# Performance work log

Hardware: AMD Instinct MI355X
Metric: run time of the kernel (lower is better)

The kernel has to match this reference:

```python
import jax, jax.numpy as jnp
import numpy as np

N, E, B = 20000, 320000, 128
IN_DIM, HID, HEADS = 64, 64, 4
D = HID * HEADS          # 256 = conv output width (concat heads)
CAT = HID + 2 * D        # 576 = dueling head input
ENC_H, DUEL_H = 512, 128
NEG_SLOPE = 0.2


def setup_inputs() -> dict:
    key = jax.random.key(0)
    ks = jax.random.split(key, 30)
    g = lambda i, shape: jax.random.normal(ks[i], shape, dtype=jnp.float32) * 0.05
    return {
        "x": jax.random.normal(ks[0], (N, IN_DIM), dtype=jnp.float32),
        "edge_index": jax.random.randint(ks[1], (2, E), 0, N, dtype=jnp.int32),
        "indices": jax.random.randint(ks[2], (B,), 0, N, dtype=jnp.int32),
        # encoder MLP: input_dim -> 512 -> hidden_dim
        "enc_w1": g(3, (IN_DIM, ENC_H)), "enc_b1": g(4, (ENC_H,)),
        "enc_w2": g(5, (ENC_H, HID)),   "enc_b2": g(6, (HID,)),
        # GATv2 conv1: HID -> HID per head, HEADS heads
        "wl1": g(7, (HID, D)),  "bl1": g(8, (D,)),
        "wr1": g(9, (HID, D)),  "br1": g(10, (D,)),
        "att1": g(11, (HEADS, HID)), "bias1": g(12, (D,)),
        # GATv2 conv2: D -> HID per head, HEADS heads
        "wl2": g(13, (D, D)),   "bl2": g(14, (D,)),
        "wr2": g(15, (D, D)),   "br2": g(16, (D,)),
        "att2": g(17, (HEADS, HID)), "bias2": g(18, (D,)),
        # dueling heads: CAT -> 128 -> {2, 1}
        "q_w1": g(19, (CAT, DUEL_H)), "q_b1": g(20, (DUEL_H,)),
        "q_w2": g(21, (DUEL_H, 2)),   "q_b2": g(22, (2,)),
        "v_w1": g(23, (CAT, DUEL_H)), "v_b1": g(24, (DUEL_H,)),
        "v_w2": g(25, (DUEL_H, 1)),   "v_b2": g(26, (1,)),
    }


def _gatv2(h, src, dst, wl, bl, wr, br, att, bias):
    # PyG GATv2Conv: e_ij = att . leaky_relu(Wl h_j + Wr h_i); softmax over
    # incoming edges of each target i; out_i = sum_j alpha_ij * (Wl h_j).
    xl = (h @ wl + bl).reshape(-1, HEADS, HID)  # source transform
    xr = (h @ wr + br).reshape(-1, HEADS, HID)  # target transform
    e = jax.nn.leaky_relu(xl[src] + xr[dst], NEG_SLOPE)      # [E', H, D]
    score = jnp.einsum('ehd,hd->eh', e, att)                 # [E', H]
    m = jax.ops.segment_max(score, dst, num_segments=N)      # stable softmax
    ex = jnp.exp(score - m[dst])
    denom = jax.ops.segment_sum(ex, dst, num_segments=N)
    alpha = ex / (denom[dst] + 1e-16)                        # [E', H]
    out = jax.ops.segment_sum(alpha[:, :, None] * xl[src], dst, num_segments=N)
    return out.reshape(-1, D) + bias


def _forward(x, edge_index, indices,
             enc_w1, enc_b1, enc_w2, enc_b2,
             wl1, bl1, wr1, br1, att1, bias1,
             wl2, bl2, wr2, br2, att2, bias2,
             q_w1, q_b1, q_w2, q_b2, v_w1, v_b1, v_w2, v_b2):
    loops = jnp.arange(N, dtype=edge_index.dtype)  # add_self_loops=True
    src = jnp.concatenate([edge_index[0], loops])
    dst = jnp.concatenate([edge_index[1], loops])

    h = jax.nn.relu(x @ enc_w1 + enc_b1)
    h = jax.nn.relu(h @ enc_w2 + enc_b2)          # encoder + F.relu
    x1 = h[indices]
    h = jax.nn.relu(_gatv2(h, src, dst, wl1, bl1, wr1, br1, att1, bias1))
    x2 = h[indices]
    h = jax.nn.relu(_gatv2(h, src, dst, wl2, bl2, wr2, br2, att2, bias2))
    x3 = h[indices]

    feat = jnp.concatenate([x1, x2, x3], axis=1)  # [B, CAT]
    q = jax.nn.relu(feat @ q_w1 + q_b1) @ q_w2 + q_b2  # [B, 2]
    v = jax.nn.relu(feat @ v_w1 + v_b1) @ v_w2 + v_b2  # [B, 1]
    return q - q.mean(axis=1, keepdims=True) + v


def reference(x, edge_index, indices,
              enc_w1, enc_b1, enc_w2, enc_b2,
              wl1, bl1, wr1, br1, att1, bias1,
              wl2, bl2, wr2, br2, att2, bias2,
              q_w1, q_b1, q_w2, q_b2, v_w1, v_b1, v_w2, v_b2):
    return _forward(x, edge_index, indices,
                    enc_w1, enc_b1, enc_w2, enc_b2,
                    wl1, bl1, wr1, br1, att1, bias1,
                    wl2, bl2, wr2, br2, att2, bias2,
                    q_w1, q_b1, q_w2, q_b2, v_w1, v_b1, v_w2, v_b2)
```

## Files before the change

kernel.cpp:

```cpp
#include <hip/hip_runtime.h>

#define IN_DIM 64
#define HID 64
#define HEADS 4
#define DD 256
#define ENC_H 512
#define DUEL_H 128
#define NEG_SLOPE 0.2f
#define WCAP 8192
#define ECAP 64

typedef _Float16 f16;
typedef __attribute__((ext_vector_type(2))) _Float16 f16x2;
typedef __attribute__((ext_vector_type(4))) _Float16 f16x4;
typedef __attribute__((ext_vector_type(8))) _Float16 f16x8;
typedef __attribute__((ext_vector_type(4))) float f32x4;

__device__ __forceinline__ f16x2 u2h(unsigned u) {
    union { unsigned u; f16x2 h; } c; c.u = u; return c.h;
}
__device__ __forceinline__ unsigned h2u(f16x2 h) {
    union { unsigned u; f16x2 h; } c; c.h = h; return c.u;
}


__global__ void prep_all(
    const float4* __restrict__ x, f16x4* __restrict__ x16, int nx4,
    const float* __restrict__ w1, const float* __restrict__ w2,
    const float* __restrict__ wl1, const float* __restrict__ wr1,
    const float* __restrict__ wl2, const float* __restrict__ wr2,
    f16* __restrict__ w1t, f16* __restrict__ w2t,
    f16* __restrict__ wcat1, f16* __restrict__ wcat2,
    f16* __restrict__ wr2nt,
    int* __restrict__ zeros, int nz) {
    int i = blockIdx.x * blockDim.x + threadIdx.x;
    if (i < nx4) {
        float4 v = x[i];
        f16x4 o = {(f16)v.x, (f16)v.y, (f16)v.z, (f16)v.w};
        x16[i] = o;
        return;
    }
    i -= nx4;
    if (i < 229376) {
        if (i < 32768) {
            int k = i >> 9, n = i & 511;
            w1t[n * 64 + k] = (f16)w1[i];
        } else if (i < 65536) {
            int j = i - 32768; int k = j >> 6, n = j & 63;
            w2t[n * 512 + k] = (f16)w2[j];
        } else if (i < 81920) {
            int j = i - 65536; int k = j >> 8, n = j & 255;
            wcat1[n * 64 + k] = (f16)wl1[j];
        } else if (i < 98304) {
            int j = i - 81920; int k = j >> 8, n = j & 255;
            wcat1[(256 + n) * 64 + k] = (f16)wr1[j];
        } else if (i < 163840) {
            int j = i - 98304; int k = j >> 8, n = j & 255;
            wcat2[n * 256 + k] = (f16)wl2[j];
        } else {
            int j = i - 163840;
            wr2nt[j] = (f16)wr2[j];
        }
        return;
    }
    i -= 229376;
    if (i < nz) zeros[i] = 0;
}


template <int K, int BN>
struct GemmCfg {
    static constexpr int SB = K + 8;
    static constexpr int CE = BN / 2 + 8;
    static constexpr int SLABSZ = BN * SB;
    static constexpr int EPISZ = 4 * 32 * CE;
    static constexpr int SMEMSZ = SLABSZ > EPISZ ? SLABSZ : EPISZ;
};

template <int K, int BN>
__device__ __forceinline__ void gemm_body(
    int bx, int by, f16* __restrict__ smem,
    const f16* __restrict__ A, const f16* __restrict__ Bt,
    const float* __restrict__ biasA, const float* __restrict__ biasB, int NS,
    int M, int relu,
    f16* __restrict__ C1, f16* __restrict__ C2) {
    constexpr int KS = K / 32;
    constexpr int PF = (KS < 8) ? KS : 8;
    constexpr int COLW = BN / 2;
    constexpr int NT = COLW / 16;
    constexpr int SB = GemmCfg<K, BN>::SB;
    constexpr int CE = GemmCfg<K, BN>::CE;

    f16* Bs = smem;
    int tid = threadIdx.x;
    int wave = tid >> 6, lane = tid & 63;
    int quad = lane >> 4, l16 = lane & 15;
    int wr = wave >> 1, wc = wave & 1;
    int row0 = by * 64;
    int col0 = bx * BN;

    constexpr int NCH = BN * K / 8;
#pragma unroll
    for (int i = 0; i < NCH / 256; ++i) {
        int c = tid + i * 256;
        int r = c / (K / 8), ko = (c % (K / 8)) * 8;
        uint4 v = *(const uint4*)&Bt[(size_t)(col0 + r) * K + ko];
        *(uint4*)&Bs[r * SB + ko] = v;
    }
    __syncthreads();

    const f16* Aptr[2];
#pragma unroll
    for (int mt = 0; mt < 2; ++mt) {
        int arow = row0 + wr * 32 + mt * 16 + l16;
        if (arow >= M) arow = M - 1;
        Aptr[mt] = &A[(size_t)arow * K + quad * 8];
    }

    f32x4 acc[2][NT];
#pragma unroll
    for (int mt = 0; mt < 2; ++mt)
#pragma unroll
        for (int j = 0; j < NT; ++j) acc[mt][j] = (f32x4){0.f, 0.f, 0.f, 0.f};

    f16x8 afb[2][PF];
#pragma unroll
    for (int mt = 0; mt < 2; ++mt)
#pragma unroll
        for (int i = 0; i < PF; ++i)
            afb[mt][i] = *(const f16x8*)&Aptr[mt][i * 32];

#pragma unroll
    for (int s = 0; s < KS; ++s) {
        f16x8 af0 = afb[0][s % PF], af1 = afb[1][s % PF];
        if (s + PF < KS) {
            afb[0][s % PF] = *(const f16x8*)&Aptr[0][(s + PF) * 32];
            afb[1][s % PF] = *(const f16x8*)&Aptr[1][(s + PF) * 32];
        }
        const f16* bbase = &Bs[(size_t)(wc * COLW) * SB + s * 32 + quad * 8];
#pragma unroll
        for (int nt = 0; nt < NT; ++nt) {
            f16x8 bf = *(const f16x8*)&bbase[(nt * 16 + l16) * SB];
            acc[0][nt] = __builtin_amdgcn_mfma_f32_16x16x32_f16(af0, bf, acc[0][nt], 0, 0, 0);
            acc[1][nt] = __builtin_amdgcn_mfma_f32_16x16x32_f16(af1, bf, acc[1][nt], 0, 0, 0);
        }
    }

    __syncthreads();
    f16* ep = &smem[wave * 32 * CE];
#pragma unroll
    for (int mt = 0; mt < 2; ++mt)
#pragma unroll
        for (int nt = 0; nt < NT; ++nt) {
            int gcol = col0 + wc * COLW + nt * 16 + l16;
            float bb = (gcol < NS) ? biasA[gcol] : biasB[gcol - NS];
#pragma unroll
            for (int r = 0; r < 4; ++r) {
                float v = acc[mt][nt][r] + bb;
                if (relu) v = fmaxf(v, 0.f);
                ep[(mt * 16 + quad * 4 + r) * CE + nt * 16 + l16] = (f16)v;
            }
        }
    constexpr int CPR = COLW / 8;
    constexpr int NPASS = (32 * CPR) / 64;
#pragma unroll
    for (int i = 0; i < NPASS; ++i) {
        int u = lane + i * 64;
        int row = u / CPR, seg = u % CPR;
        uint4 v = *(const uint4*)&ep[row * CE + seg * 8];
        int grow = row0 + wr * 32 + row;
        int gcol = col0 + wc * COLW + seg * 8;
        if (grow < M) {
            if (gcol < NS) *(uint4*)&C1[(size_t)grow * NS + gcol] = v;
            else           *(uint4*)&C2[(size_t)grow * NS + (gcol - NS)] = v;
        }
    }
}


__global__ __launch_bounds__(256) void conv2t_gather_kernel(
    const f16* __restrict__ A, const f16* __restrict__ Bt,
    const float* __restrict__ bias,
    const int* __restrict__ wlist, const int* __restrict__ wcnt,
    f16* __restrict__ C) {
    constexpr int K = 256, BN = 128;
    constexpr int KS = K / 32, PF = 8;
    constexpr int COLW = BN / 2, NT = COLW / 16;
    constexpr int SB = GemmCfg<K, BN>::SB;
    constexpr int CE = GemmCfg<K, BN>::CE;
    __shared__ __align__(16) f16 smem[GemmCfg<K, BN>::SMEMSZ];

    int M_c = wcnt[0];
    int row0 = blockIdx.y * 64;
    if (row0 >= M_c) return;

    f16* Bs = smem;
    int tid = threadIdx.x;
    int wave = tid >> 6, lane = tid & 63;
    int quad = lane >> 4, l16 = lane & 15;
    int wr = wave >> 1, wc = wave & 1;
    int col0 = blockIdx.x * BN;

    constexpr int NCH = BN * K / 8;
#pragma unroll
    for (int i = 0; i < NCH / 256; ++i) {
        int c = tid + i * 256;
        int r = c / (K / 8), ko = (c % (K / 8)) * 8;
        uint4 v = *(const uint4*)&Bt[(size_t)(col0 + r) * K + ko];
        *(uint4*)&Bs[r * SB + ko] = v;
    }
    __syncthreads();

    const f16* Aptr[2];
#pragma unroll
    for (int mt = 0; mt < 2; ++mt) {
        int crow = row0 + wr * 32 + mt * 16 + l16;
        if (crow >= M_c) crow = M_c - 1;
        int arow = wlist[crow];
        Aptr[mt] = &A[(size_t)arow * K + quad * 8];
    }

    f32x4 acc[2][NT];
#pragma unroll
    for (int mt = 0; mt < 2; ++mt)
#pragma unroll
        for (int j = 0; j < NT; ++j) acc[mt][j] = (f32x4){0.f, 0.f, 0.f, 0.f};

    f16x8 afb[2][PF];
#pragma unroll
    for (int mt = 0; mt < 2; ++mt)
#pragma unroll
        for (int i = 0; i < PF; ++i)
            afb[mt][i] = *(const f16x8*)&Aptr[mt][i * 32];

#pragma unroll
    for (int s = 0; s < KS; ++s) {
        f16x8 af0 = afb[0][s % PF], af1 = afb[1][s % PF];
        const f16* bbase = &Bs[(size_t)(wc * COLW) * SB + s * 32 + quad * 8];
#pragma unroll
        for (int nt = 0; nt < NT; ++nt) {
            f16x8 bf = *(const f16x8*)&bbase[(nt * 16 + l16) * SB];
            acc[0][nt] = __builtin_amdgcn_mfma_f32_16x16x32_f16(af0, bf, acc[0][nt], 0, 0, 0);
            acc[1][nt] = __builtin_amdgcn_mfma_f32_16x16x32_f16(af1, bf, acc[1][nt], 0, 0, 0);
        }
    }

    __syncthreads();
    f16* ep = &smem[wave * 32 * CE];
#pragma unroll
    for (int mt = 0; mt < 2; ++mt)
#pragma unroll
        for (int nt = 0; nt < NT; ++nt) {
            int gcol = col0 + wc * COLW + nt * 16 + l16;
            float bb = bias[gcol];
#pragma unroll
            for (int r = 0; r < 4; ++r)
                ep[(mt * 16 + quad * 4 + r) * CE + nt * 16 + l16] =
                    (f16)(acc[mt][nt][r] + bb);
        }
    constexpr int CPR = COLW / 8;
    constexpr int NPASS = (32 * CPR) / 64;
#pragma unroll
    for (int i = 0; i < NPASS; ++i) {
        int u = lane + i * 64;
        int row = u / CPR, seg = u % CPR;
        uint4 v = *(const uint4*)&ep[row * CE + seg * 8];
        int grow = row0 + wr * 32 + row;
        int gcol = col0 + wc * COLW + seg * 8;
        if (grow < M_c) *(uint4*)&C[(size_t)grow * DD + gcol] = v;
    }
}


__device__ __forceinline__ void wappend(int src, int* __restrict__ inW,
                                        int* __restrict__ wcnt,
                                        int* __restrict__ wlist,
                                        int* __restrict__ mapv,
                                        int* __restrict__ w_edges,
                                        int* __restrict__ ecnt) {
    if (atomicExch(&inW[src], 1) == 0) {
        int c = atomicAdd(wcnt, 1);
        if (c < WCAP) {
            wlist[c] = src;
            mapv[src] = c;
            w_edges[c * ECAP] = src;
            ecnt[c] = 1;
        }
    }
}

__global__ __launch_bounds__(256) void enc1_s0_kernel(
    const f16* __restrict__ A, const f16* __restrict__ Bt,
    const float* __restrict__ bias, int M, f16* __restrict__ C, int gemmBlocks,
    const int* __restrict__ indices, int B,
    int* __restrict__ s0f, int* __restrict__ inW, int* __restrict__ wcnt,
    int* __restrict__ wlist, int* __restrict__ mapv,
    int* __restrict__ w_edges, int* __restrict__ ecnt) {
    __shared__ __align__(16) f16 smem[GemmCfg<64, 128>::SMEMSZ];
    int bid = blockIdx.x;
    if (bid >= gemmBlocks) {
        int t = threadIdx.x;
        if (t < B) {
            int src = indices[t];
            s0f[src] = 1;
            wappend(src, inW, wcnt, wlist, mapv, w_edges, ecnt);
        }
        return;
    }
    gemm_body<64, 128>(bid & 3, bid >> 2, smem, A, Bt, bias, bias, 512, M, 1, C, C);
}

__global__ __launch_bounds__(256) void enc2_wscan_kernel(
    const f16* __restrict__ A, const f16* __restrict__ Bt,
    const float* __restrict__ bias, int M, f16* __restrict__ C, int gemmBlocks,
    const int* __restrict__ ei, int E,
    const int* __restrict__ s0f, int* __restrict__ inW, int* __restrict__ wcnt,
    int* __restrict__ wlist, int* __restrict__ mapv,
    int* __restrict__ w_edges, int* __restrict__ ecnt) {
    __shared__ __align__(16) f16 smem[GemmCfg<512, 64>::SMEMSZ];
    int bid = blockIdx.x;
    if (bid < gemmBlocks) {
        gemm_body<512, 64>(0, bid, smem, A, Bt, bias, bias, 64, M, 1, C, C);
    } else {
        int e = (bid - gemmBlocks) * 256 + threadIdx.x;
        if (e < E) {
            int dst = ei[E + e];
            if (s0f[dst])
                wappend(ei[e], inW, wcnt, wlist, mapv, w_edges, ecnt);
        }
    }
}

__global__ __launch_bounds__(256) void conv1t_ebuild_kernel(
    const f16* __restrict__ A, const f16* __restrict__ Bt,
    const float* __restrict__ biasA, const float* __restrict__ biasB, int M,
    f16* __restrict__ C1, f16* __restrict__ C2, int gemmBlocks,
    const int* __restrict__ ei, int E,
    const int* __restrict__ inW, const int* __restrict__ mapv,
    int* __restrict__ w_edges, int* __restrict__ ecnt) {
    __shared__ __align__(16) f16 smem[GemmCfg<64, 128>::SMEMSZ];
    int bid = blockIdx.x;
    if (bid < gemmBlocks) {
        gemm_body<64, 128>(bid & 3, bid >> 2, smem, A, Bt, biasA, biasB, DD, M, 0, C1, C2);
    } else {
        int e = (bid - gemmBlocks) * 256 + threadIdx.x;
        if (e < E) {
            int dst = ei[E + e];
            if (inW[dst]) {
                int c = mapv[dst];
                int pos = atomicAdd(&ecnt[c], 1);
                if (pos < ECAP) w_edges[c * ECAP + pos] = ei[e];
            }
        }
    }
}


__global__ __launch_bounds__(256) void gat_fused_kernel(
    const uint4* __restrict__ xl, const uint4* __restrict__ xr,
    const float4* __restrict__ att,
    const int* __restrict__ wlist, const int* __restrict__ wcnt,
    const int* __restrict__ w_edges, const int* __restrict__ ecnt,
    const float4* __restrict__ bias, uint4* __restrict__ h16) {
    int w = (blockIdx.x * blockDim.x + threadIdx.x) >> 6;
    int lane = threadIdx.x & 63;
    int half = lane >> 5, l32 = lane & 31;
    if (w >= wcnt[0]) return;
    int node = wlist[w];
    int L = ecnt[w];
    if (L > ECAP) L = ECAP;
    const int* elist = &w_edges[w * ECAP];
    uint4 xrw = xr[(size_t)node * 32 + l32];
    f16x2 xr0 = u2h(xrw.x), xr1 = u2h(xrw.y), xr2 = u2h(xrw.z), xr3 = u2h(xrw.w);
    float4 awA = att[l32 * 2], awB = att[l32 * 2 + 1];
    f16x2 a6[4] = {{(f16)(0.6f * awA.x), (f16)(0.6f * awA.y)},
                   {(f16)(0.6f * awA.z), (f16)(0.6f * awA.w)},
                   {(f16)(0.6f * awB.x), (f16)(0.6f * awB.y)},
                   {(f16)(0.6f * awB.z), (f16)(0.6f * awB.w)}};
    f16x2 a4[4] = {{(f16)(0.4f * awA.x), (f16)(0.4f * awA.y)},
                   {(f16)(0.4f * awA.z), (f16)(0.4f * awA.w)},
                   {(f16)(0.4f * awB.x), (f16)(0.4f * awB.y)},
                   {(f16)(0.4f * awB.z), (f16)(0.4f * awB.w)}};
    float denom = 0.f;
    float acc0 = 0.f, acc1 = 0.f, acc2 = 0.f, acc3 = 0.f;
    float acc4 = 0.f, acc5 = 0.f, acc6 = 0.f, acc7 = 0.f;

    auto edge_dot = [&](uint4 raw) -> float {
        f16x2 t0 = u2h(raw.x) + xr0, t1 = u2h(raw.y) + xr1;
        f16x2 t2 = u2h(raw.z) + xr2, t3 = u2h(raw.w) + xr3;
        float d = __builtin_amdgcn_fdot2(t0, a6[0], 0.f, false);
        d = __builtin_amdgcn_fdot2(u2h(h2u(t0) & 0x7FFF7FFFu), a4[0], d, false);
        d = __builtin_amdgcn_fdot2(t1, a6[1], d, false);
        d = __builtin_amdgcn_fdot2(u2h(h2u(t1) & 0x7FFF7FFFu), a4[1], d, false);
        d = __builtin_amdgcn_fdot2(t2, a6[2], d, false);
        d = __builtin_amdgcn_fdot2(u2h(h2u(t2) & 0x7FFF7FFFu), a4[2], d, false);
        d = __builtin_amdgcn_fdot2(t3, a6[3], d, false);
        d = __builtin_amdgcn_fdot2(u2h(h2u(t3) & 0x7FFF7FFFu), a4[3], d, false);
        return d;
    };
    auto accum = [&](uint4 raw, float ee) {
        f16x2 v0 = u2h(raw.x), v1 = u2h(raw.y), v2 = u2h(raw.z), v3 = u2h(raw.w);
        acc0 = fmaf(ee, (float)v0.x, acc0); acc1 = fmaf(ee, (float)v0.y, acc1);
        acc2 = fmaf(ee, (float)v1.x, acc2); acc3 = fmaf(ee, (float)v1.y, acc3);
        acc4 = fmaf(ee, (float)v2.x, acc4); acc5 = fmaf(ee, (float)v2.y, acc5);
        acc6 = fmaf(ee, (float)v3.x, acc6); acc7 = fmaf(ee, (float)v3.y, acc7);
    };

    int p = half;
    for (; p + 6 < L; p += 8) {
        uint4 raw[4];
#pragma unroll
        for (int j = 0; j < 4; ++j)
            raw[j] = xl[(size_t)elist[p + j * 2] * 32 + l32];
        float sc[4];
#pragma unroll
        for (int j = 0; j < 4; ++j) sc[j] = edge_dot(raw[j]);
#pragma unroll
        for (int j = 0; j < 4; ++j) sc[j] += __shfl_xor(sc[j], 1);
#pragma unroll
        for (int j = 0; j < 4; ++j) sc[j] += __shfl_xor(sc[j], 2);
#pragma unroll
        for (int j = 0; j < 4; ++j) sc[j] += __shfl_xor(sc[j], 4);
#pragma unroll
        for (int j = 0; j < 4; ++j) {
            float ee = __expf(sc[j]);
            denom += ee;
            accum(raw[j], ee);
        }
    }
    for (; p < L; p += 2) {
        uint4 raw = xl[(size_t)elist[p] * 32 + l32];
        float d = edge_dot(raw);
        d += __shfl_xor(d, 1);
        d += __shfl_xor(d, 2);
        d += __shfl_xor(d, 4);
        float ee = __expf(d);
        denom += ee;
        accum(raw, ee);
    }
    denom += __shfl_xor(denom, 32);
    acc0 += __shfl_xor(acc0, 32); acc1 += __shfl_xor(acc1, 32);
    acc2 += __shfl_xor(acc2, 32); acc3 += __shfl_xor(acc3, 32);
    acc4 += __shfl_xor(acc4, 32); acc5 += __shfl_xor(acc5, 32);
    acc6 += __shfl_xor(acc6, 32); acc7 += __shfl_xor(acc7, 32);

    if (half == 0) {
        float inv = 1.f / (denom + 1e-16f);
        float4 bbA = bias[l32 * 2], bbB = bias[l32 * 2 + 1];
        float o0 = fmaxf(fmaf(acc0, inv, bbA.x), 0.f);
        float o1 = fmaxf(fmaf(acc1, inv, bbA.y), 0.f);
        float o2 = fmaxf(fmaf(acc2, inv, bbA.z), 0.f);
        float o3 = fmaxf(fmaf(acc3, inv, bbA.w), 0.f);
        float o4 = fmaxf(fmaf(acc4, inv, bbB.x), 0.f);
        float o5 = fmaxf(fmaf(acc5, inv, bbB.y), 0.f);
        float o6 = fmaxf(fmaf(acc6, inv, bbB.z), 0.f);
        float o7 = fmaxf(fmaf(acc7, inv, bbB.w), 0.f);
        f16x2 h0 = {(f16)o0, (f16)o1}, h1 = {(f16)o2, (f16)o3};
        f16x2 h2 = {(f16)o4, (f16)o5}, h3 = {(f16)o6, (f16)o7};
        uint4 outw = make_uint4(h2u(h0), h2u(h1), h2u(h2), h2u(h3));
        h16[(size_t)node * 32 + l32] = outw;
    }
}


__global__ __launch_bounds__(1024) void gat2_head_kernel(
    const uint4* __restrict__ xl, const f16* __restrict__ hC1,
    const f16* __restrict__ wr2nt, const float* __restrict__ br2,
    const float4* __restrict__ att,
    const int* __restrict__ indices, const int* __restrict__ mapv,
    const int* __restrict__ w_edges, const int* __restrict__ ecnt,
    const float* __restrict__ bias2, const f16* __restrict__ hE16,
    const float* __restrict__ qw1, const float* __restrict__ qb1,
    const float* __restrict__ qw2, const float* __restrict__ qb2,
    const float* __restrict__ vw1, const float* __restrict__ vb1,
    const float* __restrict__ vw2, const float* __restrict__ vb2,
    float* __restrict__ out) {
    __shared__ float feat[576];
    __shared__ float xrs[256];
    __shared__ float partial[4][256];
    __shared__ float pden[16][32];
    __shared__ float pacc[16][32][8];
    __shared__ float red[384];
    int b = blockIdx.x;
    int t = threadIdx.x;
    int wave = t >> 6, lane = t & 63;
    int half = lane >> 5, l32 = lane & 31;
    int node = indices[b];

    if (t < 320) {
        feat[t] = (t < 64) ? (float)hE16[(size_t)node * 64 + t]
                           : (float)hC1[(size_t)node * 256 + t - 64];
    }
    __syncthreads();

    {
        int o = t & 255, kq = t >> 8;
        const f16* w = &wr2nt[(size_t)(kq * 64) * 256 + o];
        const float* f = &feat[64 + kq * 64];
        float a0 = 0.f, a1 = 0.f;
#pragma unroll
        for (int k = 0; k < 64; k += 2) {
            a0 = fmaf(f[k],     (float)w[(size_t)k * 256],       a0);
            a1 = fmaf(f[k + 1], (float)w[(size_t)(k + 1) * 256], a1);
        }
        partial[kq][o] = a0 + a1;
    }
    __syncthreads();
    if (t < 256)
        xrs[t] = partial[0][t] + partial[1][t] + partial[2][t] + partial[3][t] + br2[t];
    __syncthreads();

    f16x2 xr0 = {(f16)xrs[l32 * 8 + 0], (f16)xrs[l32 * 8 + 1]};
    f16x2 xr1 = {(f16)xrs[l32 * 8 + 2], (f16)xrs[l32 * 8 + 3]};
    f16x2 xr2 = {(f16)xrs[l32 * 8 + 4], (f16)xrs[l32 * 8 + 5]};
    f16x2 xr3 = {(f16)xrs[l32 * 8 + 6], (f16)xrs[l32 * 8 + 7]};

    int cidx0 = mapv[node];
    int L = ecnt[cidx0];
    if (L > ECAP) L = ECAP;
    const int* elist = &w_edges[cidx0 * ECAP];
    float4 awA = att[l32 * 2], awB = att[l32 * 2 + 1];
    f16x2 a6[4] = {{(f16)(0.6f * awA.x), (f16)(0.6f * awA.y)},
                   {(f16)(0.6f * awA.z), (f16)(0.6f * awA.w)},
                   {(f16)(0.6f * awB.x), (f16)(0.6f * awB.y)},
                   {(f16)(0.6f * awB.z), (f16)(0.6f * awB.w)}};
    f16x2 a4[4] = {{(f16)(0.4f * awA.x), (f16)(0.4f * awA.y)},
                   {(f16)(0.4f * awA.z), (f16)(0.4f * awA.w)},
                   {(f16)(0.4f * awB.x), (f16)(0.4f * awB.y)},
                   {(f16)(0.4f * awB.z), (f16)(0.4f * awB.w)}};
    float denom = 0.f;
    float acc0 = 0.f, acc1 = 0.f, acc2 = 0.f, acc3 = 0.f;
    float acc4 = 0.f, acc5 = 0.f, acc6 = 0.f, acc7 = 0.f;

    auto edge_dot = [&](uint4 raw) -> float {
        f16x2 t0 = u2h(raw.x) + xr0, t1 = u2h(raw.y) + xr1;
        f16x2 t2 = u2h(raw.z) + xr2, t3 = u2h(raw.w) + xr3;
        float d = __builtin_amdgcn_fdot2(t0, a6[0], 0.f, false);
        d = __builtin_amdgcn_fdot2(u2h(h2u(t0) & 0x7FFF7FFFu), a4[0], d, false);
        d = __builtin_amdgcn_fdot2(t1, a6[1], d, false);
        d = __builtin_amdgcn_fdot2(u2h(h2u(t1) & 0x7FFF7FFFu), a4[1], d, false);
        d = __builtin_amdgcn_fdot2(t2, a6[2], d, false);
        d = __builtin_amdgcn_fdot2(u2h(h2u(t2) & 0x7FFF7FFFu), a4[2], d, false);
        d = __builtin_amdgcn_fdot2(t3, a6[3], d, false);
        d = __builtin_amdgcn_fdot2(u2h(h2u(t3) & 0x7FFF7FFFu), a4[3], d, false);
        return d;
    };
    auto accum = [&](uint4 raw, float ee) {
        f16x2 v0 = u2h(raw.x), v1 = u2h(raw.y), v2 = u2h(raw.z), v3 = u2h(raw.w);
        acc0 = fmaf(ee, (float)v0.x, acc0); acc1 = fmaf(ee, (float)v0.y, acc1);
        acc2 = fmaf(ee, (float)v1.x, acc2); acc3 = fmaf(ee, (float)v1.y, acc3);
        acc4 = fmaf(ee, (float)v2.x, acc4); acc5 = fmaf(ee, (float)v2.y, acc5);
        acc6 = fmaf(ee, (float)v3.x, acc6); acc7 = fmaf(ee, (float)v3.y, acc7);
    };

    for (int p = (wave << 1) + half; p < L; p += 32) {
        int cidx = mapv[elist[p]];
        uint4 raw = xl[(size_t)cidx * 32 + l32];
        float d = edge_dot(raw);
        d += __shfl_xor(d, 1);
        d += __shfl_xor(d, 2);
        d += __shfl_xor(d, 4);
        float ee = __expf(d);
        denom += ee;
        accum(raw, ee);
    }
    denom += __shfl_xor(denom, 32);
    acc0 += __shfl_xor(acc0, 32); acc1 += __shfl_xor(acc1, 32);
    acc2 += __shfl_xor(acc2, 32); acc3 += __shfl_xor(acc3, 32);
    acc4 += __shfl_xor(acc4, 32); acc5 += __shfl_xor(acc5, 32);
    acc6 += __shfl_xor(acc6, 32); acc7 += __shfl_xor(acc7, 32);
    if (half == 0) {
        pden[wave][l32] = denom;
        pacc[wave][l32][0] = acc0; pacc[wave][l32][1] = acc1;
        pacc[wave][l32][2] = acc2; pacc[wave][l32][3] = acc3;
        pacc[wave][l32][4] = acc4; pacc[wave][l32][5] = acc5;
        pacc[wave][l32][6] = acc6; pacc[wave][l32][7] = acc7;
    }
    __syncthreads();

    if (t < 256) {
        int lw = t >> 3, d = t & 7;
        float den = 0.f, a = 0.f;
#pragma unroll
        for (int w = 0; w < 16; ++w) { den += pden[w][lw]; a += pacc[w][lw][d]; }
        float inv = 1.f / (den + 1e-16f);
        feat[320 + t] = fmaxf(fmaf(a, inv, bias2[t]), 0.f);
    }
    __syncthreads();

    {
        int o = t & 255, kq = t >> 8;
        int k0 = kq * 144;
        float a0 = 0.f, a1 = 0.f;
        if (o < 128) {
            const float* w = &qw1[(size_t)k0 * 128 + o];
            const float* f = &feat[k0];
#pragma unroll
            for (int k = 0; k < 144; k += 2) {
                a0 = fmaf(f[k],     w[(size_t)k * 128],       a0);
                a1 = fmaf(f[k + 1], w[(size_t)(k + 1) * 128], a1);
            }
        } else {
            const float* w = &vw1[(size_t)k0 * 128 + (o - 128)];
            const float* f = &feat[k0];
#pragma unroll
            for (int k = 0; k < 144; k += 2) {
                a0 = fmaf(f[k],     w[(size_t)k * 128],       a0);
                a1 = fmaf(f[k + 1], w[(size_t)(k + 1) * 128], a1);
            }
        }
        partial[kq][o] = a0 + a1;
    }
    __syncthreads();
    if (t < 256) {
        float s4 = partial[0][t] + partial[1][t] + partial[2][t] + partial[3][t];
        if (t < 128) {
            float aq = fmaxf(s4 + qb1[t], 0.f);
            red[t]       = aq * qw2[t * 2 + 0];
            red[128 + t] = aq * qw2[t * 2 + 1];
        } else {
            int tv = t - 128;
            float av = fmaxf(s4 + vb1[tv], 0.f);
            red[256 + tv] = av * vw2[tv];
        }
    }
    __syncthreads();
    for (int s2 = 64; s2 > 0; s2 >>= 1) {
        if (t < s2) {
            red[t] += red[t + s2];
            red[128 + t] += red[128 + t + s2];
            red[256 + t] += red[256 + t + s2];
        }
        __syncthreads();
    }
    if (t == 0) {
        float q0 = red[0] + qb2[0];
        float q1 = red[128] + qb2[1];
        float v  = red[256] + vb2[0];
        float mean = 0.5f * (q0 + q1);
        out[b * 2 + 0] = q0 - mean + v;
        out[b * 2 + 1] = q1 - mean + v;
    }
}


extern "C" void kernel_launch(void* const* d_in, const int* in_sizes, int n_in,
                              void* d_out, int out_size, void* d_ws, size_t ws_size,
                              hipStream_t stream) {
    const float* x      = (const float*)d_in[0];
    const int*   ei     = (const int*)d_in[1];
    const int*   indices= (const int*)d_in[2];
    const float* enc_w1 = (const float*)d_in[3];
    const float* enc_b1 = (const float*)d_in[4];
    const float* enc_w2 = (const float*)d_in[5];
    const float* enc_b2 = (const float*)d_in[6];
    const float* wl1    = (const float*)d_in[7];
    const float* bl1    = (const float*)d_in[8];
    const float* wr1    = (const float*)d_in[9];
    const float* br1    = (const float*)d_in[10];
    const float* att1   = (const float*)d_in[11];
    const float* bias1  = (const float*)d_in[12];
    const float* wl2    = (const float*)d_in[13];
    const float* bl2    = (const float*)d_in[14];
    const float* wr2    = (const float*)d_in[15];
    const float* br2    = (const float*)d_in[16];
    const float* att2   = (const float*)d_in[17];
    const float* bias2  = (const float*)d_in[18];
    const float* qw1    = (const float*)d_in[19];
    const float* qb1    = (const float*)d_in[20];
    const float* qw2    = (const float*)d_in[21];
    const float* qb2    = (const float*)d_in[22];
    const float* vw1    = (const float*)d_in[23];
    const float* vb1    = (const float*)d_in[24];
    const float* vw2    = (const float*)d_in[25];
    const float* vb2    = (const float*)d_in[26];

    const int N = in_sizes[0] / IN_DIM;
    const int E = in_sizes[1] / 2;
    const int B = in_sizes[2];

    char* wsb = (char*)d_ws;
    size_t off = 0;
    auto alloc = [&](size_t bytes) -> void* {
        void* p = wsb + off;
        off = (off + bytes + 255) & ~(size_t)255;
        return p;
    };
    f16* x16     = (f16*)alloc((size_t)N * 64 * 2);
    f16* h1_16   = (f16*)alloc((size_t)N * 512 * 2);
    f16* hE16    = (f16*)alloc((size_t)N * 64 * 2);
    f16* xl16    = (f16*)alloc((size_t)N * 256 * 2);
    f16* xr16    = (f16*)alloc((size_t)N * 256 * 2);
    f16* hC1_16  = (f16*)alloc((size_t)N * 256 * 2);
    f16* w1t     = (f16*)alloc((size_t)ENC_H * IN_DIM * 2);
    f16* w2t     = (f16*)alloc((size_t)HID * ENC_H * 2);
    f16* wcat1   = (f16*)alloc((size_t)512 * HID * 2);
    f16* wcat2   = (f16*)alloc((size_t)512 * DD * 2);
    f16* wr2nt   = (f16*)alloc((size_t)DD * DD * 2);
    int* zeros   = (int*)alloc((size_t)(2 * N + 16) * 4);
    int* s0f     = zeros;
    int* inW     = s0f + N;
    int* wcnt    = inW + N;
    int* wlist   = (int*)alloc((size_t)WCAP * 4);
    int* mapv    = (int*)alloc((size_t)N * 4);
    int* ecnt    = (int*)alloc((size_t)WCAP * 4);
    int* w_edges = (int*)alloc((size_t)WCAP * ECAP * 4);

    int nx4 = N * 16;
    int nz = 2 * N + 16;
    int ntot = nx4 + 229376 + nz;
    prep_all<<<(ntot + 255) / 256, 256, 0, stream>>>(
        (const float4*)x, (f16x4*)x16, nx4,
        enc_w1, enc_w2, wl1, wr1, wl2, wr2,
        w1t, w2t, wcat1, wcat2, wr2nt, zeros, nz);

    int grows = (N + 63) / 64;
    int gemmB1 = 4 * grows;
    int escanB = (E + 255) / 256;

    enc1_s0_kernel<<<gemmB1 + 1, 256, 0, stream>>>(
        x16, w1t, enc_b1, N, h1_16, gemmB1,
        indices, B, s0f, inW, wcnt, wlist, mapv, w_edges, ecnt);

    enc2_wscan_kernel<<<grows + escanB, 256, 0, stream>>>(
        h1_16, w2t, enc_b2, N, hE16, grows,
        ei, E, s0f, inW, wcnt, wlist, mapv, w_edges, ecnt);

    conv1t_ebuild_kernel<<<gemmB1 + escanB, 256, 0, stream>>>(
        hE16, wcat1, bl1, br1, N, xl16, xr16, gemmB1,
        ei, E, inW, mapv, w_edges, ecnt);

    gat_fused_kernel<<<(WCAP * 64) / 256, 256, 0, stream>>>(
        (const uint4*)xl16, (const uint4*)xr16, (const float4*)att1,
        wlist, wcnt, w_edges, ecnt, (const float4*)bias1, (uint4*)hC1_16);

    conv2t_gather_kernel<<<dim3(2, WCAP / 64), dim3(256), 0, stream>>>(
        hC1_16, wcat2, bl2, wlist, wcnt, xl16);

    gat2_head_kernel<<<B, 1024, 0, stream>>>(
        (const uint4*)xl16, hC1_16, wr2nt, br2, (const float4*)att2,
        indices, mapv, w_edges, ecnt, bias2, hE16,
        qw1, qb1, qw2, qb2, vw1, vb1, vw2, vb2, (float*)d_out);
}
```

Measured before the change: 180.8 us.

## Fold weight and input fp16 conversion into GEMM kernels, drop prep kernel

Removes the separate prep kernel that converted x and all weight matrices to transposed fp16. Each GEMM now loads fp32 weights directly, converting and transposing them into shared memory. The first encoder GEMM reads fp32 x and converts it on the fly, and a memset replaces the zeroing. This saves a launch and a full pass over x, at the cost of redundant per-block weight conversion and scattered 2-byte LDS stores.

```diff
diff --git a/kernel.cpp b/kernel.cpp
--- a/kernel.cpp
+++ b/kernel.cpp
@@ -24,50 +24,6 @@
 }
 
 
-__global__ void prep_all(
-    const float4* __restrict__ x, f16x4* __restrict__ x16, int nx4,
-    const float* __restrict__ w1, const float* __restrict__ w2,
-    const float* __restrict__ wl1, const float* __restrict__ wr1,
-    const float* __restrict__ wl2, const float* __restrict__ wr2,
-    f16* __restrict__ w1t, f16* __restrict__ w2t,
-    f16* __restrict__ wcat1, f16* __restrict__ wcat2,
-    f16* __restrict__ wr2nt,
-    int* __restrict__ zeros, int nz) {
-    int i = blockIdx.x * blockDim.x + threadIdx.x;
-    if (i < nx4) {
-        float4 v = x[i];
-        f16x4 o = {(f16)v.x, (f16)v.y, (f16)v.z, (f16)v.w};
-        x16[i] = o;
-        return;
-    }
-    i -= nx4;
-    if (i < 229376) {
-        if (i < 32768) {
-            int k = i >> 9, n = i & 511;
-            w1t[n * 64 + k] = (f16)w1[i];
-        } else if (i < 65536) {
-            int j = i - 32768; int k = j >> 6, n = j & 63;
-            w2t[n * 512 + k] = (f16)w2[j];
-        } else if (i < 81920) {
-            int j = i - 65536; int k = j >> 8, n = j & 255;
-            wcat1[n * 64 + k] = (f16)wl1[j];
-        } else if (i < 98304) {
-            int j = i - 81920; int k = j >> 8, n = j & 255;
-            wcat1[(256 + n) * 64 + k] = (f16)wr1[j];
-        } else if (i < 163840) {
-            int j = i - 98304; int k = j >> 8, n = j & 255;
-            wcat2[n * 256 + k] = (f16)wl2[j];
-        } else {
-            int j = i - 163840;
-            wr2nt[j] = (f16)wr2[j];
-        }
-        return;
-    }
-    i -= 229376;
-    if (i < nz) zeros[i] = 0;
-}
-
-
 template <int K, int BN>
 struct GemmCfg {
     static constexpr int SB = K + 8;
@@ -77,10 +33,12 @@
     static constexpr int SMEMSZ = SLABSZ > EPISZ ? SLABSZ : EPISZ;
 };
 
-template <int K, int BN>
-__device__ __forceinline__ void gemm_body(
+template <int K, int BN, bool AF32>
+__device__ __forceinline__ void gemm_body2(
     int bx, int by, f16* __restrict__ smem,
-    const f16* __restrict__ A, const f16* __restrict__ Bt,
+    const void* __restrict__ Av,
+    const float* __restrict__ wA, int strideA,
+    const float* __restrict__ wB, int strideB, int NSW,
     const float* __restrict__ biasA, const float* __restrict__ biasB, int NS,
     int M, int relu,
     f16* __restrict__ C1, f16* __restrict__ C2) {
@@ -99,23 +57,46 @@
     int row0 = by * 64;
     int col0 = bx * BN;
 
-    constexpr int NCH = BN * K / 8;
-#pragma unroll
-    for (int i = 0; i < NCH / 256; ++i) {
-        int c = tid + i * 256;
-        int r = c / (K / 8), ko = (c % (K / 8)) * 8;
-        uint4 v = *(const uint4*)&Bt[(size_t)(col0 + r) * K + ko];
-        *(uint4*)&Bs[r * SB + ko] = v;
-    }
-    __syncthreads();
-
-    const f16* Aptr[2];
+    constexpr int C4 = BN / 4;
+    constexpr int NIT = (BN * K / 4) / 256;
+#pragma unroll
+    for (int i = 0; i < NIT; ++i) {
+        int idx = tid + i * 256;
+        int c4 = idx % C4, k = idx / C4;
+        int gc = col0 + c4 * 4;
+        const float* src = (gc < NSW) ? &wA[(size_t)k * strideA + gc]
+                                      : &wB[(size_t)k * strideB + (gc - NSW)];
+        float4 v = *(const float4*)src;
+        int cb = c4 * 4;
+        Bs[(cb + 0) * SB + k] = (f16)v.x;
+        Bs[(cb + 1) * SB + k] = (f16)v.y;
+        Bs[(cb + 2) * SB + k] = (f16)v.z;
+        Bs[(cb + 3) * SB + k] = (f16)v.w;
+    }
+    __syncthreads();
+
+    const f16* A16 = (const f16*)Av;
+    const float* A32 = (const float*)Av;
+    const f16* Aptr16[2];
+    const float* Aptr32[2];
 #pragma unroll
     for (int mt = 0; mt < 2; ++mt) {
         int arow = row0 + wr * 32 + mt * 16 + l16;
         if (arow >= M) arow = M - 1;
-        Aptr[mt] = &A[(size_t)arow * K + quad * 8];
-    }
+        if constexpr (AF32) Aptr32[mt] = &A32[(size_t)arow * K + quad * 8];
+        else                Aptr16[mt] = &A16[(size_t)arow * K + quad * 8];
+    }
+    auto ldA = [&](int mt, int off) -> f16x8 {
+        if constexpr (AF32) {
+            const float* p = Aptr32[mt] + off;
+            float4 a = *(const float4*)p, b = *(const float4*)(p + 4);
+            f16x8 r = {(f16)a.x, (f16)a.y, (f16)a.z, (f16)a.w,
+                       (f16)b.x, (f16)b.y, (f16)b.z, (f16)b.w};
+            return r;
+        } else {
+            return *(const f16x8*)(Aptr16[mt] + off);
+        }
+    };
 
     f32x4 acc[2][NT];
 #pragma unroll
@@ -128,14 +109,14 @@
     for (int mt = 0; mt < 2; ++mt)
 #pragma unroll
         for (int i = 0; i < PF; ++i)
-            afb[mt][i] = *(const f16x8*)&Aptr[mt][i * 32];
+            afb[mt][i] = ldA(mt, i * 32);
 
 #pragma unroll
     for (int s = 0; s < KS; ++s) {
         f16x8 af0 = afb[0][s % PF], af1 = afb[1][s % PF];
         if (s + PF < KS) {
-            afb[0][s % PF] = *(const f16x8*)&Aptr[0][(s + PF) * 32];
-            afb[1][s % PF] = *(const f16x8*)&Aptr[1][(s + PF) * 32];
+            afb[0][s % PF] = ldA(0, (s + PF) * 32);
+            afb[1][s % PF] = ldA(1, (s + PF) * 32);
         }
         const f16* bbase = &Bs[(size_t)(wc * COLW) * SB + s * 32 + quad * 8];
 #pragma unroll
@@ -179,7 +160,7 @@
 
 
 __global__ __launch_bounds__(256) void conv2t_gather_kernel(
-    const f16* __restrict__ A, const f16* __restrict__ Bt,
+    const f16* __restrict__ A, const float* __restrict__ wl2,
     const float* __restrict__ bias,
     const int* __restrict__ wlist, const int* __restrict__ wcnt,
     f16* __restrict__ C) {
@@ -201,13 +182,18 @@
     int wr = wave >> 1, wc = wave & 1;
     int col0 = blockIdx.x * BN;
 
-    constexpr int NCH = BN * K / 8;
-#pragma unroll
-    for (int i = 0; i < NCH / 256; ++i) {
-        int c = tid + i * 256;
-        int r = c / (K / 8), ko = (c % (K / 8)) * 8;
-        uint4 v = *(const uint4*)&Bt[(size_t)(col0 + r) * K + ko];
-        *(uint4*)&Bs[r * SB + ko] = v;
+    constexpr int C4 = BN / 4;
+    constexpr int NIT = (BN * K / 4) / 256;
+#pragma unroll
+    for (int i = 0; i < NIT; ++i) {
+        int idx = tid + i * 256;
+        int c4 = idx % C4, k = idx / C4;
+        float4 v = *(const float4*)&wl2[(size_t)k * 256 + col0 + c4 * 4];
+        int cb = c4 * 4;
+        Bs[(cb + 0) * SB + k] = (f16)v.x;
+        Bs[(cb + 1) * SB + k] = (f16)v.y;
+        Bs[(cb + 2) * SB + k] = (f16)v.z;
+        Bs[(cb + 3) * SB + k] = (f16)v.w;
     }
     __syncthreads();
 
@@ -290,7 +276,7 @@
 }
 
 __global__ __launch_bounds__(256) void enc1_s0_kernel(
-    const f16* __restrict__ A, const f16* __restrict__ Bt,
+    const float* __restrict__ x, const float* __restrict__ w1,
     const float* __restrict__ bias, int M, f16* __restrict__ C, int gemmBlocks,
     const int* __restrict__ indices, int B,
     int* __restrict__ s0f, int* __restrict__ inW, int* __restrict__ wcnt,
@@ -307,11 +293,13 @@
         }
         return;
     }
-    gemm_body<64, 128>(bid & 3, bid >> 2, smem, A, Bt, bias, bias, 512, M, 1, C, C);
+    gemm_body2<64, 128, true>(bid & 3, bid >> 2, smem, x,
+                              w1, 512, w1, 512, 4096,
+                              bias, bias, 512, M, 1, C, C);
 }
 
 __global__ __launch_bounds__(256) void enc2_wscan_kernel(
-    const f16* __restrict__ A, const f16* __restrict__ Bt,
+    const f16* __restrict__ A, const float* __restrict__ w2,
     const float* __restrict__ bias, int M, f16* __restrict__ C, int gemmBlocks,
     const int* __restrict__ ei, int E,
     const int* __restrict__ s0f, int* __restrict__ inW, int* __restrict__ wcnt,
@@ -320,7 +308,9 @@
     __shared__ __align__(16) f16 smem[GemmCfg<512, 64>::SMEMSZ];
     int bid = blockIdx.x;
     if (bid < gemmBlocks) {
-        gemm_body<512, 64>(0, bid, smem, A, Bt, bias, bias, 64, M, 1, C, C);
+        gemm_body2<512, 64, false>(0, bid, smem, A,
+                                   w2, 64, w2, 64, 4096,
+                                   bias, bias, 64, M, 1, C, C);
     } else {
         int e = (bid - gemmBlocks) * 256 + threadIdx.x;
         if (e < E) {
@@ -332,7 +322,8 @@
 }
 
 __global__ __launch_bounds__(256) void conv1t_ebuild_kernel(
-    const f16* __restrict__ A, const f16* __restrict__ Bt,
+    const f16* __restrict__ A,
+    const float* __restrict__ wl1, const float* __restrict__ wr1,
     const float* __restrict__ biasA, const float* __restrict__ biasB, int M,
     f16* __restrict__ C1, f16* __restrict__ C2, int gemmBlocks,
     const int* __restrict__ ei, int E,
@@ -341,7 +332,9 @@
     __shared__ __align__(16) f16 smem[GemmCfg<64, 128>::SMEMSZ];
     int bid = blockIdx.x;
     if (bid < gemmBlocks) {
-        gemm_body<64, 128>(bid & 3, bid >> 2, smem, A, Bt, biasA, biasB, DD, M, 0, C1, C2);
+        gemm_body2<64, 128, false>(bid & 3, bid >> 2, smem, A,
+                                   wl1, 256, wr1, 256, 256,
+                                   biasA, biasB, DD, M, 0, C1, C2);
     } else {
         int e = (bid - gemmBlocks) * 256 + threadIdx.x;
         if (e < E) {
@@ -465,7 +458,7 @@
 
 __global__ __launch_bounds__(1024) void gat2_head_kernel(
     const uint4* __restrict__ xl, const f16* __restrict__ hC1,
-    const f16* __restrict__ wr2nt, const float* __restrict__ br2,
+    const float* __restrict__ wr2, const float* __restrict__ br2,
     const float4* __restrict__ att,
     const int* __restrict__ indices, const int* __restrict__ mapv,
     const int* __restrict__ w_edges, const int* __restrict__ ecnt,
@@ -495,13 +488,13 @@
 
     {
         int o = t & 255, kq = t >> 8;
-        const f16* w = &wr2nt[(size_t)(kq * 64) * 256 + o];
+        const float* w = &wr2[(size_t)(kq * 64) * 256 + o];
         const float* f = &feat[64 + kq * 64];
         float a0 = 0.f, a1 = 0.f;
 #pragma unroll
         for (int k = 0; k < 64; k += 2) {
-            a0 = fmaf(f[k],     (float)w[(size_t)k * 256],       a0);
-            a1 = fmaf(f[k + 1], (float)w[(size_t)(k + 1) * 256], a1);
+            a0 = fmaf(f[k],     (float)(f16)w[(size_t)k * 256],       a0);
+            a1 = fmaf(f[k + 1], (float)(f16)w[(size_t)(k + 1) * 256], a1);
         }
         partial[kq][o] = a0 + a1;
     }
@@ -686,17 +679,11 @@
         off = (off + bytes + 255) & ~(size_t)255;
         return p;
     };
-    f16* x16     = (f16*)alloc((size_t)N * 64 * 2);
     f16* h1_16   = (f16*)alloc((size_t)N * 512 * 2);
     f16* hE16    = (f16*)alloc((size_t)N * 64 * 2);
     f16* xl16    = (f16*)alloc((size_t)N * 256 * 2);
     f16* xr16    = (f16*)alloc((size_t)N * 256 * 2);
     f16* hC1_16  = (f16*)alloc((size_t)N * 256 * 2);
-    f16* w1t     = (f16*)alloc((size_t)ENC_H * IN_DIM * 2);
-    f16* w2t     = (f16*)alloc((size_t)HID * ENC_H * 2);
-    f16* wcat1   = (f16*)alloc((size_t)512 * HID * 2);
-    f16* wcat2   = (f16*)alloc((size_t)512 * DD * 2);
-    f16* wr2nt   = (f16*)alloc((size_t)DD * DD * 2);
     int* zeros   = (int*)alloc((size_t)(2 * N + 16) * 4);
     int* s0f     = zeros;
     int* inW     = s0f + N;
@@ -706,28 +693,24 @@
     int* ecnt    = (int*)alloc((size_t)WCAP * 4);
     int* w_edges = (int*)alloc((size_t)WCAP * ECAP * 4);
 
-    int nx4 = N * 16;
     int nz = 2 * N + 16;
-    int ntot = nx4 + 229376 + nz;
-    prep_all<<<(ntot + 255) / 256, 256, 0, stream>>>(
-        (const float4*)x, (f16x4*)x16, nx4,
-        enc_w1, enc_w2, wl1, wr1, wl2, wr2,
-        w1t, w2t, wcat1, wcat2, wr2nt, zeros, nz);
+
+    hipMemsetAsync(zeros, 0, (size_t)nz * 4, stream);
 
     int grows = (N + 63) / 64;
     int gemmB1 = 4 * grows;
     int escanB = (E + 255) / 256;
 
     enc1_s0_kernel<<<gemmB1 + 1, 256, 0, stream>>>(
-        x16, w1t, enc_b1, N, h1_16, gemmB1,
+        x, enc_w1, enc_b1, N, h1_16, gemmB1,
         indices, B, s0f, inW, wcnt, wlist, mapv, w_edges, ecnt);
 
     enc2_wscan_kernel<<<grows + escanB, 256, 0, stream>>>(
-        h1_16, w2t, enc_b2, N, hE16, grows,
+        h1_16, enc_w2, enc_b2, N, hE16, grows,
         ei, E, s0f, inW, wcnt, wlist, mapv, w_edges, ecnt);
 
     conv1t_ebuild_kernel<<<gemmB1 + escanB, 256, 0, stream>>>(
-        hE16, wcat1, bl1, br1, N, xl16, xr16, gemmB1,
+        hE16, wl1, wr1, bl1, br1, N, xl16, xr16, gemmB1,
         ei, E, inW, mapv, w_edges, ecnt);
 
     gat_fused_kernel<<<(WCAP * 64) / 256, 256, 0, stream>>>(
@@ -735,10 +718,10 @@
         wlist, wcnt, w_edges, ecnt, (const float4*)bias1, (uint4*)hC1_16);
 
     conv2t_gather_kernel<<<dim3(2, WCAP / 64), dim3(256), 0, stream>>>(
-        hC1_16, wcat2, bl2, wlist, wcnt, xl16);
+        hC1_16, wl2, bl2, wlist, wcnt, xl16);
 
     gat2_head_kernel<<<B, 1024, 0, stream>>>(
-        (const uint4*)xl16, hC1_16, wr2nt, br2, (const float4*)att2,
+        (const uint4*)xl16, hC1_16, wr2, br2, (const float4*)att2,
         indices, mapv, w_edges, ecnt, bias2, hE16,
         qw1, qb1, qw2, qb2, vw1, vb1, vw2, vb2, (float*)d_out);
 }
```

After: 195.3 us. +8.0%, slower.
